# Kernel tuning notes

Measured on AMD Instinct MI355X. Metric: run time of the kernel, lower is better.

Reference implementation:

```python
import jax, jax.numpy as jnp
import numpy as np

# tag2index constants
PAD, START, END, T = 0, 14, 15, 16
B, L, V, E, H = 128, 512, 30000, 256, 256


def _lstm(xs, w_ih, w_hh, b, reverse=False):
    """xs: [L, B, E] -> hs: [L, B, H]. PyTorch gate order i,f,g,o."""
    Bsz = xs.shape[1]
    Hd = w_hh.shape[1]
    def cell(carry, xt):
        h, c = carry
        g = xt @ w_ih.T + h @ w_hh.T + b  # [B, 4H]
        i, f, gg, o = jnp.split(g, 4, axis=-1)
        c = jax.nn.sigmoid(f) * c + jax.nn.sigmoid(i) * jnp.tanh(gg)
        h = jax.nn.sigmoid(o) * jnp.tanh(c)
        return (h, c), h
    init = (jnp.zeros((Bsz, Hd), xs.dtype), jnp.zeros((Bsz, Hd), xs.dtype))
    _, hs = jax.lax.scan(cell, init, xs, reverse=reverse)
    return hs


def setup_inputs() -> dict:
    key = jax.random.key(0)
    ks = jax.random.split(key, 12)
    batch_data = jax.random.randint(ks[0], (B, L), 0, V, dtype=jnp.int32)
    # variable-length tags with contiguous trailing PAD (as the model assumes)
    lengths = jax.random.randint(ks[1], (B,), L // 4, L + 1)
    raw_tags = jax.random.randint(ks[2], (B, L), 1, 14, dtype=jnp.int32)  # real tags in [1,14)
    pos = jnp.arange(L)[None, :]
    batch_tag = jnp.where(pos < lengths[:, None], raw_tags, PAD).astype(jnp.int32)
    s = 0.05
    emb = jax.random.normal(ks[3], (V, E), jnp.float32) * s
    w_ih_f = jax.random.normal(ks[4], (4 * H, E), jnp.float32) * s
    w_hh_f = jax.random.normal(ks[5], (4 * H, H), jnp.float32) * s
    b_f = jnp.zeros((4 * H,), jnp.float32)
    w_ih_b = jax.random.normal(ks[6], (4 * H, E), jnp.float32) * s
    w_hh_b = jax.random.normal(ks[7], (4 * H, H), jnp.float32) * s
    b_b = jnp.zeros((4 * H,), jnp.float32)
    w_cls = jax.random.normal(ks[8], (T, 2 * H), jnp.float32) * s
    b_cls = jnp.zeros((T,), jnp.float32)
    transition = jnp.full((T, T), 1.0 / T, jnp.float32)
    return {"batch_data": batch_data, "batch_tag": batch_tag, "emb": emb,
            "w_ih_f": w_ih_f, "w_hh_f": w_hh_f, "b_f": b_f,
            "w_ih_b": w_ih_b, "w_hh_b": w_hh_b, "b_b": b_b,
            "w_cls": w_cls, "b_cls": b_cls, "transition": transition}


def reference(batch_data, batch_tag, emb, w_ih_f, w_hh_f, b_f,
              w_ih_b, w_hh_b, b_b, w_cls, b_cls, transition):
    # ---- BiLSTM encoder ----
    x = emb[batch_data]                      # [B, L, E]
    xs = jnp.moveaxis(x, 1, 0)               # [L, B, E]
    hf = _lstm(xs, w_ih_f, w_hh_f, b_f, reverse=False)
    hb = _lstm(xs, w_ih_b, w_hh_b, b_b, reverse=True)
    out = jnp.moveaxis(jnp.concatenate([hf, hb], axis=-1), 0, 1)  # [B, L, 2H]
    emission = out @ w_cls.T + b_cls          # [B, L, T]
    crf_scores = emission[:, :, None, :] + transition[None, None]  # [B, L, T, T]

    # ---- CRF loss (linear-chain forward algorithm) ----
    mask = batch_tag != PAD                   # [B, L]
    lengths = mask.sum(axis=1)                # [B]
    prev = jnp.concatenate(
        [jnp.full((B, 1), START, batch_tag.dtype), batch_tag[:, :-1]], axis=1)
    idx = (batch_tag + prev * T).astype(jnp.int32)  # flat (prev_tag, cur_tag) index
    flat = crf_scores.reshape(B, L, T * T)
    g = jnp.take_along_axis(flat, idx[:, :, None], axis=2)[..., 0]
    golden_scores = jnp.sum(jnp.where(mask, g, 0.0))

    sc_t = jnp.moveaxis(crf_scores, 1, 0)     # [L, B, T, T]
    init = sc_t[0, :, START, :]               # [B, T] (all lengths >= 1)
    def step(prev_scores, x_t):
        sc, t = x_t
        new = jax.nn.logsumexp(sc + prev_scores[:, :, None], axis=1)  # [B, T]
        active = (lengths > t)[:, None]
        return jnp.where(active, new, prev_scores), None
    final, _ = jax.lax.scan(step, init, (sc_t[1:], jnp.arange(1, L)))
    all_path_scores = jnp.sum(final[:, END])
    loss = (all_path_scores - golden_scores) / B
    return loss
```

## Files before the change

kernel.cpp:

```cpp
#include <hip/hip_runtime.h>

#define Bsz 128
#define Lseq 512
#define Hdim 256
#define Tn 16
#define START_TAG 14
#define END_TAG 15

typedef float f32x4 __attribute__((ext_vector_type(4)));
typedef short s16x8 __attribute__((ext_vector_type(8)));

__device__ __forceinline__ unsigned short f2bf(float f) {
    unsigned int u = __builtin_bit_cast(unsigned int, f);
    u += 0x7fffu + ((u >> 16) & 1u);
    return (unsigned short)(u >> 16);
}
__device__ __forceinline__ float bf2f(unsigned int bits16) {
    return __builtin_bit_cast(float, bits16 << 16);
}
__device__ __forceinline__ float sigmoidf_(float x) {
    return 1.0f / (1.0f + __expf(-x));
}

__global__ void embprep_kernel(const float* __restrict__ emb,
                               unsigned int* __restrict__ embb, int n2) {
    int i = blockIdx.x * blockDim.x + threadIdx.x;
    int stride = gridDim.x * blockDim.x;
    for (; i < n2; i += stride)
        embb[i] = (unsigned int)f2bf(emb[2 * i]) | ((unsigned int)f2bf(emb[2 * i + 1]) << 16);
}

__global__ void wprep_kernel(const float* __restrict__ wih_f, const float* __restrict__ whh_f,
                             const float* __restrict__ wih_b, const float* __restrict__ whh_b,
                             unsigned int* __restrict__ wtile) {
    int bid = blockIdx.x;
    int ki  = bid & 15;
    int tl  = (bid >> 4) & 3;
    int ug  = (bid >> 6) & 15;
    int dir = bid >> 10;
    int t = threadIdx.x;
    int lane = t >> 2, j = t & 3;
    int n = lane & 15, kq = lane >> 4;
    int k0 = ki * 32 + kq * 8 + 2 * j;
    int col = tl * 256 + ug * 16 + n;
    const float* wih = dir ? wih_b : wih_f;
    const float* whh = dir ? whh_b : whh_f;
    float f0, f1;
    if (k0 < 256) { f0 = wih[col * 256 + k0];       f1 = wih[col * 256 + k0 + 1]; }
    else          { f0 = whh[col * 256 + k0 - 256]; f1 = whh[col * 256 + k0 - 255]; }
    wtile[(size_t)bid * 256 + t] = (unsigned int)f2bf(f0) | ((unsigned int)f2bf(f1) << 16);
}

__global__ void lengths_kernel(const int* __restrict__ tag, int* __restrict__ lengths) {
    int b = blockIdx.x;
    int tid = threadIdx.x;
    int cnt = 0;
    for (int l = tid; l < Lseq; l += blockDim.x)
        cnt += (tag[b * Lseq + l] != 0) ? 1 : 0;
    for (int off = 32; off > 0; off >>= 1) cnt += __shfl_down(cnt, off);
    __shared__ int red[4];
    if ((tid & 63) == 0) red[tid >> 6] = cnt;
    __syncthreads();
    if (tid == 0) lengths[b] = red[0] + red[1] + red[2] + red[3];
}

__global__ __launch_bounds__(256, 1) void bilstm_persist(
    const int* __restrict__ bd,
    const unsigned int* __restrict__ embb,
    const unsigned int* __restrict__ wtile,
    const float* __restrict__ b_f, const float* __restrict__ b_b,
    const float* __restrict__ w_cls,
    float* __restrict__ em_f, float* __restrict__ em_b,
    unsigned int* __restrict__ ring,
    int* __restrict__ flags)
{
    const int wg  = blockIdx.x;
    const int dir = wg >> 7;
    const int bg  = (wg >> 4) & 7;
    const int ug  = wg & 15;
    const int grp = dir * 8 + bg;
    const int tid = threadIdx.x;
    const int gb0 = bg * 16;

    __shared__ unsigned int w_lds[16384];
    __shared__ unsigned int h_lds[16 * 132];
    __shared__ float g_lds[4][16][17];
    __shared__ float part_lds[16][17];
    __shared__ float bias_lds[64];
    __shared__ float wcls_lds[256];

    {
        const unsigned int* wsrc = wtile + ((size_t)(dir * 16 + ug) << 14);
        for (int i = 0; i < 16; ++i) {
            int idx = tid + 256 * i;
            uint4 v = *(const uint4*)(wsrc + (size_t)idx * 4);
            *(uint4*)&w_lds[idx * 4] = v;
        }
        if (tid < 64) {
            const float* bias = dir ? b_b : b_f;
            bias_lds[tid] = bias[(tid >> 4) * 256 + ug * 16 + (tid & 15)];
        }
        wcls_lds[tid] = w_cls[(size_t)ug * (2 * Hdim) + dir * Hdim + tid];
    }

    const int wv = tid >> 6;
    const int l  = tid & 63;
    const int n  = l & 15;
    const int kq = l >> 4;
    const int cb = tid >> 4, cu = tid & 15;
    const int em_m = tid >> 4, em_seg = tid & 15;
    float c_reg = 0.f;
    float* emout = dir ? em_b : em_f;
    const int* bd_row = bd + (size_t)(gb0 + n) * Lseq;

    unsigned int* rbase = ring + (size_t)dir * 2 * 16384;

    __syncthreads();

    f32x4 acc_x = {0.f, 0.f, 0.f, 0.f};
    {
        const int t0 = dir ? (Lseq - 1) : 0;
        int tok = bd_row[t0];
        const unsigned int* xsrc = embb + (size_t)tok * 128 + kq * 4;
        #pragma unroll
        for (int ki = 0; ki < 8; ++ki) {
            uint4 xv = *(const uint4*)(xsrc + ki * 16);
            s16x8 a = __builtin_bit_cast(s16x8, xv);
            s16x8 b = *(const s16x8*)&w_lds[((wv * 16 + ki) * 64 + l) * 4];
            acc_x = __builtin_amdgcn_mfma_f32_16x16x32_bf16(a, b, acc_x, 0, 0, 0);
        }
    }

    for (int s = 0; s < Lseq; ++s) {
        const int t = dir ? (Lseq - 1 - s) : s;
        const unsigned int* hprev = rbase + ((s & 1) ^ 1) * 16384;
        unsigned int*       hcur  = rbase + (s & 1) * 16384;

        {
            int m = tid >> 4, q0 = (tid & 15) * 8;
            const unsigned int* src = hprev + (gb0 + m) * 128 + q0;
            unsigned int v[8];
            #pragma unroll
            for (int j = 0; j < 8; ++j)
                v[j] = __hip_atomic_load(src + j, __ATOMIC_RELAXED, __HIP_MEMORY_SCOPE_AGENT);
            *(uint4*)&h_lds[m * 132 + q0]     = make_uint4(v[0], v[1], v[2], v[3]);
            *(uint4*)&h_lds[m * 132 + q0 + 4] = make_uint4(v[4], v[5], v[6], v[7]);
        }
        __syncthreads();

        if (s > 0) {
            const unsigned int* hr = &h_lds[em_m * 132 + em_seg * 8];
            const float* wc = &wcls_lds[em_seg * 16];
            float p = 0.f;
            #pragma unroll
            for (int j = 0; j < 8; ++j) {
                unsigned int v = hr[j];
                p += bf2f(v & 0xffffu) * wc[2 * j] + bf2f(v >> 16) * wc[2 * j + 1];
            }
            part_lds[em_m][em_seg] = p;
        }
        {
            f32x4 acc = acc_x;
            #pragma unroll
            for (int kih = 0; kih < 8; ++kih) {
                s16x8 a = *(const s16x8*)&h_lds[n * 132 + kih * 16 + kq * 4];
                s16x8 b = *(const s16x8*)&w_lds[(((wv * 16) + 8 + kih) * 64 + l) * 4];
                acc = __builtin_amdgcn_mfma_f32_16x16x32_bf16(a, b, acc, 0, 0, 0);
            }
            #pragma unroll
            for (int r = 0; r < 4; ++r)
                g_lds[wv][kq * 4 + r][n] = acc[r];
        }
        __syncthreads();

        {
            float gi = g_lds[0][cb][cu] + bias_lds[cu];
            float gf = g_lds[1][cb][cu] + bias_lds[16 + cu];
            float gg = g_lds[2][cb][cu] + bias_lds[32 + cu];
            float go = g_lds[3][cb][cu] + bias_lds[48 + cu];
            float cn = sigmoidf_(gf) * c_reg + sigmoidf_(gi) * tanhf(gg);
            c_reg = cn;
            float hn = sigmoidf_(go) * tanhf(cn);
            unsigned int hbits = (unsigned int)f2bf(hn);
            unsigned int other = (unsigned int)__shfl_down((int)hbits, 1);
            if ((cu & 1) == 0) {
                unsigned int pk = hbits | (other << 16);
                __hip_atomic_store(hcur + (gb0 + cb) * 128 + ug * 8 + (cu >> 1), pk,
                                   __ATOMIC_RELAXED, __HIP_MEMORY_SCOPE_AGENT);
            }
        }
        if (s > 0 && tid < 16) {
            float ssum = 0.f;
            #pragma unroll
            for (int q = 0; q < 16; ++q) ssum += part_lds[tid][q];
            int t_prev = dir ? (Lseq - s) : (s - 1);
            emout[((size_t)(gb0 + tid) * Lseq + t_prev) * Tn + ug] = ssum;
        }
        __syncthreads();

        if (tid == 0)
            __hip_atomic_store(&flags[((size_t)s * 16 + grp) * 16 + ug], 1,
                               __ATOMIC_RELAXED, __HIP_MEMORY_SCOPE_AGENT);

        if (s + 1 < Lseq) {
            const int tn = dir ? (Lseq - 2 - s) : (s + 1);
            int tok = bd_row[tn];
            const unsigned int* xsrc = embb + (size_t)tok * 128 + kq * 4;
            f32x4 ax = {0.f, 0.f, 0.f, 0.f};
            #pragma unroll
            for (int ki = 0; ki < 8; ++ki) {
                uint4 xv = *(const uint4*)(xsrc + ki * 16);
                s16x8 a = __builtin_bit_cast(s16x8, xv);
                s16x8 b = *(const s16x8*)&w_lds[((wv * 16 + ki) * 64 + l) * 4];
                ax = __builtin_amdgcn_mfma_f32_16x16x32_bf16(a, b, ax, 0, 0, 0);
            }
            acc_x = ax;
        }

        if (wv == 0) {
            const int* flg = &flags[((size_t)s * 16 + grp) * 16];
            while (true) {
                int v = (l < 16)
                    ? __hip_atomic_load(&flg[l], __ATOMIC_RELAXED, __HIP_MEMORY_SCOPE_AGENT)
                    : 1;
                if (__all(v != 0)) break;
                __builtin_amdgcn_s_sleep(1);
            }
        }
        __syncthreads();
    }

    {
        const unsigned int* hlast = rbase + ((Lseq - 1) & 1) * 16384;
        int m = tid >> 4, q0 = (tid & 15) * 8;
        const unsigned int* src = hlast + (gb0 + m) * 128 + q0;
        unsigned int v[8];
        #pragma unroll
        for (int j = 0; j < 8; ++j)
            v[j] = __hip_atomic_load(src + j, __ATOMIC_RELAXED, __HIP_MEMORY_SCOPE_AGENT);
        *(uint4*)&h_lds[m * 132 + q0]     = make_uint4(v[0], v[1], v[2], v[3]);
        *(uint4*)&h_lds[m * 132 + q0 + 4] = make_uint4(v[4], v[5], v[6], v[7]);
        __syncthreads();
        {
            const unsigned int* hr = &h_lds[em_m * 132 + em_seg * 8];
            const float* wc = &wcls_lds[em_seg * 16];
            float p = 0.f;
            #pragma unroll
            for (int j = 0; j < 8; ++j) {
                unsigned int vv = hr[j];
                p += bf2f(vv & 0xffffu) * wc[2 * j] + bf2f(vv >> 16) * wc[2 * j + 1];
            }
            part_lds[em_m][em_seg] = p;
        }
        __syncthreads();
        if (tid < 16) {
            float ssum = 0.f;
            #pragma unroll
            for (int q = 0; q < 16; ++q) ssum += part_lds[tid][q];
            int t_tail = dir ? 0 : (Lseq - 1);
            emout[((size_t)(gb0 + tid) * Lseq + t_tail) * Tn + ug] = ssum;
        }
    }
}

__global__ void golden_kernel(const int* __restrict__ tag,
                              const float* __restrict__ em_f,
                              const float* __restrict__ em_b,
                              const float* __restrict__ b_cls,
                              const float* __restrict__ trans,
                              float* __restrict__ golden)
{
    int b = blockIdx.x;
    int tid = threadIdx.x;
    float s = 0.f;
    for (int l = tid; l < Lseq; l += blockDim.x) {
        int tg = tag[b * Lseq + l];
        if (tg != 0) {
            int prev = (l == 0) ? START_TAG : tag[b * Lseq + l - 1];
            size_t e = ((size_t)b * Lseq + l) * Tn + tg;
            s += em_f[e] + em_b[e] + b_cls[tg] + trans[prev * Tn + tg];
        }
    }
    for (int off = 32; off > 0; off >>= 1) s += __shfl_down(s, off);
    __shared__ float red[4];
    if ((tid & 63) == 0) red[tid >> 6] = s;
    __syncthreads();
    if (tid == 0) atomicAdd(golden, red[0] + red[1] + red[2] + red[3]);
}

__global__ void crf_forward_kernel(const float* __restrict__ em_f,
                                   const float* __restrict__ em_b,
                                   const float* __restrict__ b_cls,
                                   const float* __restrict__ trans,
                                   const int* __restrict__ lengths,
                                   float* __restrict__ allpath)
{
    int b = blockIdx.x;
    int lane = threadIdx.x;
    int j = lane & 15;
    float tcol[16];
    #pragma unroll
    for (int i = 0; i < 16; ++i) tcol[i] = trans[i * Tn + j];
    float bc = b_cls[j];
    size_t e0 = ((size_t)b * Lseq) * Tn + j;
    float alpha = em_f[e0] + em_b[e0] + bc + tcol[START_TAG];
    int len = lengths[b];
    for (int t = 1; t < Lseq; ++t) {
        float av[16];
        float m = -1e30f;
        #pragma unroll
        for (int i = 0; i < 16; ++i) {
            av[i] = __shfl(alpha, i) + tcol[i];
            m = fmaxf(m, av[i]);
        }
        float sum = 0.f;
        #pragma unroll
        for (int i = 0; i < 16; ++i) sum += __expf(av[i] - m);
        size_t e = ((size_t)b * Lseq + t) * Tn + j;
        float nv = em_f[e] + em_b[e] + bc + m + __logf(sum);
        alpha = (t < len) ? nv : alpha;
    }
    if (lane == END_TAG) atomicAdd(allpath, alpha);
}

__global__ void finalize_kernel(const float* __restrict__ scal, float* __restrict__ out) {
    out[0] = (scal[1] - scal[0]) / (float)Bsz;
}

extern "C" void kernel_launch(void* const* d_in, const int* in_sizes, int n_in,
                              void* d_out, int out_size, void* d_ws, size_t ws_size,
                              hipStream_t stream)
{
    (void)in_sizes; (void)n_in; (void)out_size; (void)ws_size;
    const int*   bd     = (const int*)d_in[0];
    const int*   tag    = (const int*)d_in[1];
    const float* emb    = (const float*)d_in[2];
    const float* w_ih_f = (const float*)d_in[3];
    const float* w_hh_f = (const float*)d_in[4];
    const float* b_f    = (const float*)d_in[5];
    const float* w_ih_b = (const float*)d_in[6];
    const float* w_hh_b = (const float*)d_in[7];
    const float* b_b    = (const float*)d_in[8];
    const float* w_cls  = (const float*)d_in[9];
    const float* b_cls  = (const float*)d_in[10];
    const float* trans  = (const float*)d_in[11];
    float* out = (float*)d_out;

    float* ws = (float*)d_ws;
    float* em_f = ws;
    float* em_b = em_f + (size_t)Bsz * Lseq * Tn;
    unsigned int* ring = (unsigned int*)(em_b + (size_t)Bsz * Lseq * Tn);
    float* scal = (float*)(ring + 65536);
    int* flags = (int*)(scal + 8);
    int* lengths = flags + (size_t)Lseq * 16 * 16;
    unsigned int* wtile = (unsigned int*)(lengths + 128);
    unsigned int* embb = wtile + (size_t)524288;

    size_t zbytes = (65536 + 8 + (size_t)Lseq * 16 * 16) * 4;
    hipMemsetAsync(ring, 0, zbytes, stream);

    embprep_kernel<<<2048, 256, 0, stream>>>(emb, embb, 30000 * 128);
    wprep_kernel<<<2048, 256, 0, stream>>>(w_ih_f, w_hh_f, w_ih_b, w_hh_b, wtile);
    lengths_kernel<<<Bsz, 256, 0, stream>>>(tag, lengths);

    void* kargs[] = {
        (void*)&bd, (void*)&embb, (void*)&wtile,
        (void*)&b_f, (void*)&b_b, (void*)&w_cls,
        (void*)&em_f, (void*)&em_b,
        (void*)&ring, (void*)&flags
    };
    hipLaunchCooperativeKernel((const void*)bilstm_persist,
                               dim3(256), dim3(256), kargs, 0, stream);

    golden_kernel<<<Bsz, 256, 0, stream>>>(tag, em_f, em_b, b_cls, trans, scal);
    crf_forward_kernel<<<Bsz, 64, 0, stream>>>(em_f, em_b, b_cls, trans, lengths, scal + 1);
    finalize_kernel<<<1, 1, 0, stream>>>(scal, out);
}
```

Before: 2.346 ms.

## Replace flag-based inter-block barrier with step-tagged data words in ring

Each hidden-state word in the ring becomes 64 bits, carrying the bf16 pair plus the step index. Consumers poll the data words directly until every tag matches, instead of publishing per-block flags and waiting on them behind extra __syncthreads. This removes a flag store, a block barrier and the separate flag polling from each recurrent step, and the h values are already in registers once the wait ends. In exchange, ring traffic doubles in size and every thread spins on global atomics rather than one wave polling flags.

```diff
diff --git a/kernel.cpp b/kernel.cpp
--- a/kernel.cpp
+++ b/kernel.cpp
@@ -71,14 +71,12 @@
     const float* __restrict__ b_f, const float* __restrict__ b_b,
     const float* __restrict__ w_cls,
     float* __restrict__ em_f, float* __restrict__ em_b,
-    unsigned int* __restrict__ ring,
-    int* __restrict__ flags)
+    unsigned long long* __restrict__ ring)
 {
     const int wg  = blockIdx.x;
     const int dir = wg >> 7;
     const int bg  = (wg >> 4) & 7;
     const int ug  = wg & 15;
-    const int grp = dir * 8 + bg;
     const int tid = threadIdx.x;
     const int gb0 = bg * 16;
 
@@ -93,14 +91,15 @@
         const unsigned int* wsrc = wtile + ((size_t)(dir * 16 + ug) << 14);
         for (int i = 0; i < 16; ++i) {
             int idx = tid + 256 * i;
-            uint4 v = *(const uint4*)(wsrc + (size_t)idx * 4);
-            *(uint4*)&w_lds[idx * 4] = v;
+            uint4 v4 = *(const uint4*)(wsrc + (size_t)idx * 4);
+            *(uint4*)&w_lds[idx * 4] = v4;
         }
         if (tid < 64) {
             const float* bias = dir ? b_b : b_f;
             bias_lds[tid] = bias[(tid >> 4) * 256 + ug * 16 + (tid & 15)];
         }
         wcls_lds[tid] = w_cls[(size_t)ug * (2 * Hdim) + dir * Hdim + tid];
+        for (int i = tid; i < 16 * 132; i += 256) h_lds[i] = 0;
     }
 
     const int wv = tid >> 6;
@@ -109,11 +108,12 @@
     const int kq = l >> 4;
     const int cb = tid >> 4, cu = tid & 15;
     const int em_m = tid >> 4, em_seg = tid & 15;
+    const int hm = tid >> 4, hj0 = (tid & 15) * 8;
     float c_reg = 0.f;
     float* emout = dir ? em_b : em_f;
     const int* bd_row = bd + (size_t)(gb0 + n) * Lseq;
 
-    unsigned int* rbase = ring + (size_t)dir * 2 * 16384;
+    unsigned long long* rbase = ring + (size_t)dir * 2 * 16384;
 
     __syncthreads();
 
@@ -131,20 +131,13 @@
         }
     }
 
+    unsigned long long v[8];
+
     for (int s = 0; s < Lseq; ++s) {
-        const int t = dir ? (Lseq - 1 - s) : s;
-        const unsigned int* hprev = rbase + ((s & 1) ^ 1) * 16384;
-        unsigned int*       hcur  = rbase + (s & 1) * 16384;
-
-        {
-            int m = tid >> 4, q0 = (tid & 15) * 8;
-            const unsigned int* src = hprev + (gb0 + m) * 128 + q0;
-            unsigned int v[8];
+        if (s > 0) {
             #pragma unroll
             for (int j = 0; j < 8; ++j)
-                v[j] = __hip_atomic_load(src + j, __ATOMIC_RELAXED, __HIP_MEMORY_SCOPE_AGENT);
-            *(uint4*)&h_lds[m * 132 + q0]     = make_uint4(v[0], v[1], v[2], v[3]);
-            *(uint4*)&h_lds[m * 132 + q0 + 4] = make_uint4(v[4], v[5], v[6], v[7]);
+                h_lds[hm * 132 + hj0 + j] = (unsigned int)v[j];
         }
         __syncthreads();
 
@@ -154,8 +147,8 @@
             float p = 0.f;
             #pragma unroll
             for (int j = 0; j < 8; ++j) {
-                unsigned int v = hr[j];
-                p += bf2f(v & 0xffffu) * wc[2 * j] + bf2f(v >> 16) * wc[2 * j + 1];
+                unsigned int w = hr[j];
+                p += bf2f(w & 0xffffu) * wc[2 * j] + bf2f(w >> 16) * wc[2 * j + 1];
             }
             part_lds[em_m][em_seg] = p;
         }
@@ -184,9 +177,11 @@
             unsigned int hbits = (unsigned int)f2bf(hn);
             unsigned int other = (unsigned int)__shfl_down((int)hbits, 1);
             if ((cu & 1) == 0) {
-                unsigned int pk = hbits | (other << 16);
-                __hip_atomic_store(hcur + (gb0 + cb) * 128 + ug * 8 + (cu >> 1), pk,
-                                   __ATOMIC_RELAXED, __HIP_MEMORY_SCOPE_AGENT);
+                unsigned long long pk = (unsigned long long)(hbits | (other << 16))
+                                      | ((unsigned long long)(s + 1) << 32);
+                __hip_atomic_store(
+                    rbase + ((size_t)(s & 1) * 16384) + (size_t)(gb0 + cb) * 128 + ug * 8 + (cu >> 1),
+                    pk, __ATOMIC_RELAXED, __HIP_MEMORY_SCOPE_AGENT);
             }
         }
         if (s > 0 && tid < 16) {
@@ -196,11 +191,12 @@
             int t_prev = dir ? (Lseq - s) : (s - 1);
             emout[((size_t)(gb0 + tid) * Lseq + t_prev) * Tn + ug] = ssum;
         }
-        __syncthreads();
-
-        if (tid == 0)
-            __hip_atomic_store(&flags[((size_t)s * 16 + grp) * 16 + ug], 1,
-                               __ATOMIC_RELAXED, __HIP_MEMORY_SCOPE_AGENT);
+
+        const unsigned long long* src =
+            rbase + ((size_t)(s & 1) * 16384) + (size_t)(gb0 + hm) * 128 + hj0;
+        #pragma unroll
+        for (int j = 0; j < 8; ++j)
+            v[j] = __hip_atomic_load(src + j, __ATOMIC_RELAXED, __HIP_MEMORY_SCOPE_AGENT);
 
         if (s + 1 < Lseq) {
             const int tn = dir ? (Lseq - 2 - s) : (s + 1);
@@ -217,29 +213,28 @@
             acc_x = ax;
         }
 
-        if (wv == 0) {
-            const int* flg = &flags[((size_t)s * 16 + grp) * 16];
+        {
+            const unsigned long long want = (unsigned long long)(s + 1);
+            unsigned int pend = 0xffu;
             while (true) {
-                int v = (l < 16)
-                    ? __hip_atomic_load(&flg[l], __ATOMIC_RELAXED, __HIP_MEMORY_SCOPE_AGENT)
-                    : 1;
-                if (__all(v != 0)) break;
-                __builtin_amdgcn_s_sleep(1);
-            }
-        }
-        __syncthreads();
+                #pragma unroll
+                for (int j = 0; j < 8; ++j)
+                    if ((pend & (1u << j)) && ((v[j] >> 32) == want))
+                        pend &= ~(1u << j);
+                if (!pend) break;
+                #pragma unroll
+                for (int j = 0; j < 8; ++j)
+                    if (pend & (1u << j))
+                        v[j] = __hip_atomic_load(src + j, __ATOMIC_RELAXED,
+                                                 __HIP_MEMORY_SCOPE_AGENT);
+            }
+        }
     }
 
     {
-        const unsigned int* hlast = rbase + ((Lseq - 1) & 1) * 16384;
-        int m = tid >> 4, q0 = (tid & 15) * 8;
-        const unsigned int* src = hlast + (gb0 + m) * 128 + q0;
-        unsigned int v[8];
         #pragma unroll
         for (int j = 0; j < 8; ++j)
-            v[j] = __hip_atomic_load(src + j, __ATOMIC_RELAXED, __HIP_MEMORY_SCOPE_AGENT);
-        *(uint4*)&h_lds[m * 132 + q0]     = make_uint4(v[0], v[1], v[2], v[3]);
-        *(uint4*)&h_lds[m * 132 + q0 + 4] = make_uint4(v[4], v[5], v[6], v[7]);
+            h_lds[hm * 132 + hj0 + j] = (unsigned int)v[j];
         __syncthreads();
         {
             const unsigned int* hr = &h_lds[em_m * 132 + em_seg * 8];
@@ -349,15 +344,14 @@
     float* ws = (float*)d_ws;
     float* em_f = ws;
     float* em_b = em_f + (size_t)Bsz * Lseq * Tn;
-    unsigned int* ring = (unsigned int*)(em_b + (size_t)Bsz * Lseq * Tn);
+    unsigned long long* ring =
+        (unsigned long long*)(em_b + (size_t)Bsz * Lseq * Tn);
     float* scal = (float*)(ring + 65536);
-    int* flags = (int*)(scal + 8);
-    int* lengths = flags + (size_t)Lseq * 16 * 16;
+    int* lengths = (int*)(scal + 8);
     unsigned int* wtile = (unsigned int*)(lengths + 128);
     unsigned int* embb = wtile + (size_t)524288;
 
-    size_t zbytes = (65536 + 8 + (size_t)Lseq * 16 * 16) * 4;
-    hipMemsetAsync(ring, 0, zbytes, stream);
+    hipMemsetAsync(ring, 0, 65536 * 8 + 8 * sizeof(float), stream);
 
     embprep_kernel<<<2048, 256, 0, stream>>>(emb, embb, 30000 * 128);
     wprep_kernel<<<2048, 256, 0, stream>>>(w_ih_f, w_hh_f, w_ih_b, w_hh_b, wtile);
@@ -367,7 +361,7 @@
         (void*)&bd, (void*)&embb, (void*)&wtile,
         (void*)&b_f, (void*)&b_b, (void*)&w_cls,
         (void*)&em_f, (void*)&em_b,
-        (void*)&ring, (void*)&flags
+        (void*)&ring
     };
     hipLaunchCooperativeKernel((const void*)bilstm_persist,
                                dim3(256), dim3(256), kargs, 0, stream);
```

Result: slower. 2.749 ms (+17.2%).

## Replace group-wide barrier with per-wave fine-grained flags in persistent BiLSTM

Applied to the files above, without the earlier changes.

Each wave now publishes its own completion flag after writing its slice of h, and each thread at the next step polls only the one flag for the h segment it reads, instead of one flag per block followed by a wave-0 poll and block barriers. This removes two __syncthreads and the all-flags spin from every recurrent step, so blocks can start as soon as their needed inputs are ready. The cost is four times as much flag memory to zero and many more scattered polling loads per step. Correctness now rests on an explicit vmcnt wait before the flag store, with no release fence.

```diff
diff --git a/kernel.cpp b/kernel.cpp
--- a/kernel.cpp
+++ b/kernel.cpp
@@ -101,6 +101,7 @@
             bias_lds[tid] = bias[(tid >> 4) * 256 + ug * 16 + (tid & 15)];
         }
         wcls_lds[tid] = w_cls[(size_t)ug * (2 * Hdim) + dir * Hdim + tid];
+        for (int i = tid; i < 16 * 132; i += 256) h_lds[i] = 0;
     }
 
     const int wv = tid >> 6;
@@ -109,6 +110,7 @@
     const int kq = l >> 4;
     const int cb = tid >> 4, cu = tid & 15;
     const int em_m = tid >> 4, em_seg = tid & 15;
+    const int pm = tid >> 4, pq = tid & 15;
     float c_reg = 0.f;
     float* emout = dir ? em_b : em_f;
     const int* bd_row = bd + (size_t)(gb0 + n) * Lseq;
@@ -132,19 +134,20 @@
     }
 
     for (int s = 0; s < Lseq; ++s) {
-        const int t = dir ? (Lseq - 1 - s) : s;
-        const unsigned int* hprev = rbase + ((s & 1) ^ 1) * 16384;
-        unsigned int*       hcur  = rbase + (s & 1) * 16384;
-
-        {
-            int m = tid >> 4, q0 = (tid & 15) * 8;
-            const unsigned int* src = hprev + (gb0 + m) * 128 + q0;
+        unsigned int* hcur = rbase + (s & 1) * 16384;
+
+        if (s > 0) {
+            const int* fp = &flags[((((size_t)(s - 1) * 16 + grp) * 4 + wv) << 4) + pq];
+            while (__hip_atomic_load(fp, __ATOMIC_RELAXED, __HIP_MEMORY_SCOPE_AGENT) == 0)
+                __builtin_amdgcn_s_sleep(1);
+            const unsigned int* src = rbase + (((s - 1) & 1) ? 16384 : 0)
+                                    + (gb0 + pm) * 128 + pq * 8;
             unsigned int v[8];
             #pragma unroll
             for (int j = 0; j < 8; ++j)
                 v[j] = __hip_atomic_load(src + j, __ATOMIC_RELAXED, __HIP_MEMORY_SCOPE_AGENT);
-            *(uint4*)&h_lds[m * 132 + q0]     = make_uint4(v[0], v[1], v[2], v[3]);
-            *(uint4*)&h_lds[m * 132 + q0 + 4] = make_uint4(v[4], v[5], v[6], v[7]);
+            *(uint4*)&h_lds[pm * 132 + pq * 8]     = make_uint4(v[0], v[1], v[2], v[3]);
+            *(uint4*)&h_lds[pm * 132 + pq * 8 + 4] = make_uint4(v[4], v[5], v[6], v[7]);
         }
         __syncthreads();
 
@@ -196,10 +199,9 @@
             int t_prev = dir ? (Lseq - s) : (s - 1);
             emout[((size_t)(gb0 + tid) * Lseq + t_prev) * Tn + ug] = ssum;
         }
-        __syncthreads();
-
-        if (tid == 0)
-            __hip_atomic_store(&flags[((size_t)s * 16 + grp) * 16 + ug], 1,
+        asm volatile("s_waitcnt vmcnt(0)" ::: "memory");
+        if (l == 0)
+            __hip_atomic_store(&flags[((((size_t)s * 16 + grp) * 4 + wv) << 4) + ug], 1,
                                __ATOMIC_RELAXED, __HIP_MEMORY_SCOPE_AGENT);
 
         if (s + 1 < Lseq) {
@@ -216,30 +218,20 @@
             }
             acc_x = ax;
         }
-
-        if (wv == 0) {
-            const int* flg = &flags[((size_t)s * 16 + grp) * 16];
-            while (true) {
-                int v = (l < 16)
-                    ? __hip_atomic_load(&flg[l], __ATOMIC_RELAXED, __HIP_MEMORY_SCOPE_AGENT)
-                    : 1;
-                if (__all(v != 0)) break;
-                __builtin_amdgcn_s_sleep(1);
-            }
-        }
-        __syncthreads();
     }
 
     {
-        const unsigned int* hlast = rbase + ((Lseq - 1) & 1) * 16384;
-        int m = tid >> 4, q0 = (tid & 15) * 8;
-        const unsigned int* src = hlast + (gb0 + m) * 128 + q0;
+        const int* fp = &flags[((((size_t)(Lseq - 1) * 16 + grp) * 4 + wv) << 4) + pq];
+        while (__hip_atomic_load(fp, __ATOMIC_RELAXED, __HIP_MEMORY_SCOPE_AGENT) == 0)
+            __builtin_amdgcn_s_sleep(1);
+        const unsigned int* src = rbase + (((Lseq - 1) & 1) ? 16384 : 0)
+                                + (gb0 + pm) * 128 + pq * 8;
         unsigned int v[8];
         #pragma unroll
         for (int j = 0; j < 8; ++j)
             v[j] = __hip_atomic_load(src + j, __ATOMIC_RELAXED, __HIP_MEMORY_SCOPE_AGENT);
-        *(uint4*)&h_lds[m * 132 + q0]     = make_uint4(v[0], v[1], v[2], v[3]);
-        *(uint4*)&h_lds[m * 132 + q0 + 4] = make_uint4(v[4], v[5], v[6], v[7]);
+        *(uint4*)&h_lds[pm * 132 + pq * 8]     = make_uint4(v[0], v[1], v[2], v[3]);
+        *(uint4*)&h_lds[pm * 132 + pq * 8 + 4] = make_uint4(v[4], v[5], v[6], v[7]);
         __syncthreads();
         {
             const unsigned int* hr = &h_lds[em_m * 132 + em_seg * 8];
@@ -352,11 +344,11 @@
     unsigned int* ring = (unsigned int*)(em_b + (size_t)Bsz * Lseq * Tn);
     float* scal = (float*)(ring + 65536);
     int* flags = (int*)(scal + 8);
-    int* lengths = flags + (size_t)Lseq * 16 * 16;
+    int* lengths = flags + (size_t)Lseq * 16 * 4 * 16;
     unsigned int* wtile = (unsigned int*)(lengths + 128);
     unsigned int* embb = wtile + (size_t)524288;
 
-    size_t zbytes = (65536 + 8 + (size_t)Lseq * 16 * 16) * 4;
+    size_t zbytes = (65536 + 8 + (size_t)Lseq * 16 * 4 * 16) * 4;
     hipMemsetAsync(ring, 0, zbytes, stream);
 
     embprep_kernel<<<2048, 256, 0, stream>>>(emb, embb, 30000 * 128);
```

Result: slower. 2.441 ms (+4.1%).
